# Optimization experiments

Measured on AMD Instinct MI355X. Metric: run time of the kernel, lower is better.

The kernel has to match this reference:

```python
import jax, jax.numpy as jnp
import numpy as np

LMAX, MMAX, C = 4, 2, 128
E, N = 40000, 4000
CUTOFF, RESCALE = 12.0, 5.0
EPS = 1e-5

def _mappings(lmax, mmax):
    # l-major coefficient listing with m in [-min(l,mmax), min(l,mmax)]
    m_list = []
    for l in range(lmax + 1):
        mm = min(l, mmax)
        m_list += list(range(-mm, mm + 1))
    m_c = np.array(m_list)
    n = len(m_list)
    to_m = np.zeros((n, n), dtype=np.float32)  # m-major <- l-major permutation
    off = 0
    for m in range(mmax + 1):
        idx_r = np.where(m_c == m)[0]
        for i, j in enumerate(idx_r):
            to_m[off + i, j] = 1.0
        off += len(idx_r)
        if m > 0:
            idx_i = np.where(m_c == -m)[0]
            for i, j in enumerate(idx_i):
                to_m[off + i, j] = 1.0
            off += len(idx_i)
    full_m = np.concatenate([np.arange(-l, l + 1) for l in range(lmax + 1)])
    out_idx = np.where(np.abs(full_m) <= mmax)[0]  # out_mask as index list
    return jnp.asarray(to_m), jnp.asarray(out_idx)

TO_M, OUT_IDX = _mappings(LMAX, MMAX)
M0 = LMAX + 1            # number of m=0 coefficients (5)
M_ALL = TO_M.shape[0]    # number of |m|<=mmax coefficients (19)
NCOEF = (LMAX + 1) ** 2  # full coefficient count (25)

def setup_inputs() -> dict:
    key = jax.random.key(0)
    ks = jax.random.split(key, 8)
    return {
        "x": jax.random.normal(ks[0], (N, NCOEF, C), jnp.float32),
        "x_edge": jax.random.normal(ks[1], (E, 128), jnp.float32),
        "edge_distance": jax.random.uniform(ks[2], (E,), jnp.float32) * CUTOFF,
        "wigner_inv": jax.random.normal(ks[3], (E, NCOEF, NCOEF), jnp.float32) / np.float32(np.sqrt(NCOEF)),
        "edge_index": jax.random.randint(ks[4], (2, E), 0, N),
        "w1": jax.random.normal(ks[5], (128, 64), jnp.float32) / np.float32(np.sqrt(128.0)),
        "b1": jnp.zeros((64,), jnp.float32),
        "g1": jnp.ones((64,), jnp.float32),
        "be1": jnp.zeros((64,), jnp.float32),
        "w2": jax.random.normal(ks[6], (64, 64), jnp.float32) / 8.0,
        "b2": jnp.zeros((64,), jnp.float32),
        "g2": jnp.ones((64,), jnp.float32),
        "be2": jnp.zeros((64,), jnp.float32),
        "w3": jax.random.normal(ks[7], (64, M0 * C), jnp.float32) / 8.0,
        "b3": jnp.zeros((M0 * C,), jnp.float32),
        "node_offset": 0,
    }

def _ln(h, g, b):
    mu = jnp.mean(h, -1, keepdims=True)
    var = jnp.mean((h - mu) ** 2, -1, keepdims=True)
    return (h - mu) * jax.lax.rsqrt(var + EPS) * g + b

def _envelope(d):
    # PolynomialEnvelope with exponent p=5
    p = 5.0
    a = -(p + 1.0) * (p + 2.0) / 2.0   # -21
    bb = p * (p + 2.0)                 #  35
    c = -p * (p + 1.0) / 2.0           # -15
    env = 1.0 + a * d**5 + bb * d**6 + c * d**7
    return jnp.where(d < 1.0, env, jnp.zeros_like(d))

def reference(x, x_edge, edge_distance, wigner_inv, edge_index,
              w1, b1, g1, be1, w2, b2, g2, be2, w3, b3, node_offset):
    # RadialMLP: (Linear -> LayerNorm -> SiLU) x2 -> Linear
    h = jax.nn.silu(_ln(x_edge @ w1 + b1, g1, be1))
    h = jax.nn.silu(_ln(h @ w2 + b2, g2, be2))
    m0 = (h @ w3 + b3).reshape(-1, M0, C)               # [E, M0, C]
    # zero-padding to M_ALL rows then applying the permutation TO_M equals
    # contracting only the first M0 (m=0) rows of TO_M
    emb = jnp.einsum("nac,ab->nbc", m0, TO_M[:M0])       # [E, M_ALL, C] (l-order)
    emb = jnp.einsum("nij,njc->nic", wigner_inv[:, :, OUT_IDX], emb)  # [E, NCOEF, C]
    env = _envelope(edge_distance / CUTOFF)
    emb = emb * env[:, None, None]
    dst = edge_index[1] - node_offset
    return x.at[dst].add(emb / RESCALE)
```

## Files before the change

kernel.cpp:

```cpp
#include <hip/hip_runtime.h>
#include <cstddef>


constexpr int C_DIM   = 128;
constexpr int NCOEF   = 25;
constexpr int M0d     = 5;
constexpr float EPS_LN      = 1e-5f;
constexpr float INV_CUTOFF  = 1.0f / 12.0f;
constexpr float INV_RESCALE = 0.2f;

typedef __attribute__((ext_vector_type(8))) short short8;
typedef __attribute__((ext_vector_type(4))) short short4v;
typedef __attribute__((ext_vector_type(4))) float f32x4;

__device__ __forceinline__ short f2bf(float f) {
    unsigned u = __float_as_uint(f);
    unsigned r = u + 0x7FFFu + ((u >> 16) & 1u);
    return (short)(r >> 16);
}

__device__ __forceinline__ float silu(float z) {
    return z / (1.0f + __expf(-z));
}

__global__ __launch_bounds__(256) void prep_weights(
    const float* __restrict__ w1, const float* __restrict__ w2,
    const float* __restrict__ w3,
    short* __restrict__ w1T, short* __restrict__ w2T, short* __restrict__ w3T)
{
    int i = blockIdx.x * 256 + threadIdx.x;
    if (i < 64 * 128) {
        int n = i >> 7, k = i & 127;
        w1T[i] = f2bf(w1[k * 64 + n]);
    }
    if (i < 64 * 64) {
        int n = i >> 6, k = i & 63;
        w2T[i] = f2bf(w2[k * 64 + n]);
    }
    if (i < 640 * 64) {
        int n = i >> 6, k = i & 63;
        w3T[i] = f2bf(w3[k * 640 + n]);
    }
}

__global__ __launch_bounds__(256) void count_kernel(
    const int* __restrict__ edge_index, const int* __restrict__ noff,
    int* __restrict__ cnt, int E, int N)
{
    int e = blockIdx.x * 256 + threadIdx.x;
    if (e < E) {
        int d = edge_index[E + e] - noff[0];
        if (d >= 0 && d < N) atomicAdd(&cnt[d], 1);
    }
}

__global__ __launch_bounds__(256) void scan_kernel(
    const int* __restrict__ cnt, int* __restrict__ offs, int N)
{
    __shared__ int s_wsum[4];
    const int t = threadIdx.x;
    const int lane = t & 63, w = t >> 6;
    const int chunk = (N + 255) / 256;
    const int base = t * chunk;

    int s = 0;
    for (int j = 0; j < chunk; ++j)
        if (base + j < N) s += cnt[base + j];

    int v = s;
    #pragma unroll
    for (int off = 1; off < 64; off <<= 1) {
        int u = __shfl_up(v, off, 64);
        if (lane >= off) v += u;
    }
    if (lane == 63) s_wsum[w] = v;
    __syncthreads();
    int wbase = 0;
    for (int k = 0; k < w; ++k) wbase += s_wsum[k];
    int run = wbase + v - s;

    if (t == 0) offs[0] = 0;
    for (int j = 0; j < chunk; ++j) {
        if (base + j < N) {
            run += cnt[base + j];
            offs[base + j + 1] = run;
        }
    }
}

__global__ __launch_bounds__(256) void fill_kernel(
    const int* __restrict__ edge_index, const int* __restrict__ noff,
    const int* __restrict__ offs, int* __restrict__ cur,
    int* __restrict__ ipos, int E, int N)
{
    int e = blockIdx.x * 256 + threadIdx.x;
    if (e < E) {
        int d = edge_index[E + e] - noff[0];
        if (d >= 0 && d < N) {
            int p = atomicAdd(&cur[d], 1);
            ipos[e] = offs[d] + p;
        }
    }
}

__global__ __launch_bounds__(256) void compact_kernel(
    const float* __restrict__ wigner_inv,
    const int*   __restrict__ ipos,
    unsigned short* __restrict__ wkT,
    int E)
{
    __shared__ float s_raw[16 * 625];
    __shared__ int   s_ipos[16];

    const int t  = threadIdx.x;
    const int g0 = blockIdx.x * 16;
    const int nloc = (E - g0) < 16 ? (E - g0) : 16;

    if (t < nloc) s_ipos[t] = ipos[g0 + t];

    if (nloc == 16) {
        const float4* src = (const float4*)(wigner_inv + (size_t)g0 * 625);
        #pragma unroll 4
        for (int f = t; f < 2500; f += 256)
            *(float4*)&s_raw[f * 4] = src[f];
    } else {
        const float* src = wigner_inv + (size_t)g0 * 625;
        for (int f = t; f < nloc * 625; f += 256)
            s_raw[f] = src[f];
    }
    __syncthreads();

    const int total = nloc * 160;
    #pragma unroll 4
    for (int f = t; f < total; f += 256) {
        int el = f / 160;
        int r  = f - el * 160;
        int a  = r >> 5;
        int i  = r & 31;
        int ip = s_ipos[el];
        if ((unsigned)ip < (unsigned)E) {
            unsigned short v = 0;
            if (i < 25) v = (unsigned short)f2bf(s_raw[el * 625 + i * 25 + a * (a + 1)]);
            wkT[((size_t)ip * 5 + a) * 32 + i] = v;
        }
    }
}

__global__ __launch_bounds__(256) void mlp_mfma_kernel(
    const float* __restrict__ x_edge,
    const float* __restrict__ edge_distance,
    const int*   __restrict__ ipos,
    const short* __restrict__ w1T,
    const float* __restrict__ b1,
    const float* __restrict__ g1, const float* __restrict__ be1,
    const short* __restrict__ w2T,
    const float* __restrict__ b2,
    const float* __restrict__ g2, const float* __restrict__ be2,
    const short* __restrict__ w3T,
    const float* __restrict__ b3,
    unsigned short* __restrict__ m0p,
    int E)
{
    __shared__ short s_h[4][1024];

    const int t  = threadIdx.x;
    const int w  = t >> 6;
    const int l  = t & 63;
    const int e16 = l & 15;
    const int g   = l >> 4;
    const int g0  = blockIdx.x * 64;
    const int row = g0 + w * 16 + e16;
    const int rowc = row < E ? row : (E - 1);
    const bool valid = row < E;
    const int swz = (e16 & 7) << 4;

    char* lds = (char*)&s_h[w][0];

    float sc;
    {
        float d  = edge_distance[rowc] * INV_CUTOFF;
        float d2 = d * d;
        float d5 = d2 * d2 * d;
        float env = 1.0f + d5 * (-21.0f + d * (35.0f + d * (-15.0f)));
        sc = ((d < 1.0f) ? env : 0.0f) * INV_RESCALE;
    }
    const int ip = valid ? ipos[rowc] : 0;
    const bool ipok = valid && ((unsigned)ip < (unsigned)E);

    short8 bx[4];
    {
        const float* xr = x_edge + (size_t)rowc * C_DIM + 8 * g;
        #pragma unroll
        for (int kt = 0; kt < 4; ++kt) {
            float4 f0 = *(const float4*)(xr + kt * 32);
            float4 f1 = *(const float4*)(xr + kt * 32 + 4);
            short8 v;
            v[0] = f2bf(f0.x); v[1] = f2bf(f0.y); v[2] = f2bf(f0.z); v[3] = f2bf(f0.w);
            v[4] = f2bf(f1.x); v[5] = f2bf(f1.y); v[6] = f2bf(f1.z); v[7] = f2bf(f1.w);
            bx[kt] = v;
        }
    }

    f32x4 acc1[4];
    #pragma unroll
    for (int nt = 0; nt < 4; ++nt) {
        float4 bv = *(const float4*)(b1 + nt * 16 + 4 * g);
        f32x4 acc = {bv.x, bv.y, bv.z, bv.w};
        #pragma unroll
        for (int kt = 0; kt < 4; ++kt) {
            short8 aw = *(const short8*)(w1T + (nt * 16 + e16) * 128 + kt * 32 + 8 * g);
            acc = __builtin_amdgcn_mfma_f32_16x16x32_bf16(aw, bx[kt], acc, 0, 0, 0);
        }
        acc1[nt] = acc;
    }

    {
        float s = 0.0f;
        #pragma unroll
        for (int nt = 0; nt < 4; ++nt)
            s += acc1[nt][0] + acc1[nt][1] + acc1[nt][2] + acc1[nt][3];
        s += __shfl_xor(s, 16);
        s += __shfl_xor(s, 32);
        float mu = s * (1.0f / 64.0f);
        float q = 0.0f;
        #pragma unroll
        for (int nt = 0; nt < 4; ++nt) {
            #pragma unroll
            for (int r = 0; r < 4; ++r) {
                float d = acc1[nt][r] - mu;
                q += d * d;
            }
        }
        q += __shfl_xor(q, 16);
        q += __shfl_xor(q, 32);
        float rstd = rsqrtf(q * (1.0f / 64.0f) + EPS_LN);
        #pragma unroll
        for (int nt = 0; nt < 4; ++nt) {
            float4 gv = *(const float4*)(g1 + nt * 16 + 4 * g);
            float4 bv = *(const float4*)(be1 + nt * 16 + 4 * g);
            short4v hv;
            hv[0] = f2bf(silu((acc1[nt][0] - mu) * rstd * gv.x + bv.x));
            hv[1] = f2bf(silu((acc1[nt][1] - mu) * rstd * gv.y + bv.y));
            hv[2] = f2bf(silu((acc1[nt][2] - mu) * rstd * gv.z + bv.z));
            hv[3] = f2bf(silu((acc1[nt][3] - mu) * rstd * gv.w + bv.w));
            *(short4v*)(lds + e16 * 128 + ((nt * 32 + 8 * g) ^ swz)) = hv;
        }
    }
    asm volatile("s_waitcnt lgkmcnt(0)" ::: "memory");

    short8 bh[2];
    #pragma unroll
    for (int kt = 0; kt < 2; ++kt)
        bh[kt] = *(const short8*)(lds + e16 * 128 + ((kt * 64 + 16 * g) ^ swz));

    f32x4 acc2[4];
    #pragma unroll
    for (int nt = 0; nt < 4; ++nt) {
        float4 bv = *(const float4*)(b2 + nt * 16 + 4 * g);
        f32x4 acc = {bv.x, bv.y, bv.z, bv.w};
        #pragma unroll
        for (int kt = 0; kt < 2; ++kt) {
            short8 aw = *(const short8*)(w2T + (nt * 16 + e16) * 64 + kt * 32 + 8 * g);
            acc = __builtin_amdgcn_mfma_f32_16x16x32_bf16(aw, bh[kt], acc, 0, 0, 0);
        }
        acc2[nt] = acc;
    }

    {
        float s = 0.0f;
        #pragma unroll
        for (int nt = 0; nt < 4; ++nt)
            s += acc2[nt][0] + acc2[nt][1] + acc2[nt][2] + acc2[nt][3];
        s += __shfl_xor(s, 16);
        s += __shfl_xor(s, 32);
        float mu = s * (1.0f / 64.0f);
        float q = 0.0f;
        #pragma unroll
        for (int nt = 0; nt < 4; ++nt) {
            #pragma unroll
            for (int r = 0; r < 4; ++r) {
                float d = acc2[nt][r] - mu;
                q += d * d;
            }
        }
        q += __shfl_xor(q, 16);
        q += __shfl_xor(q, 32);
        float rstd = rsqrtf(q * (1.0f / 64.0f) + EPS_LN);
        #pragma unroll
        for (int nt = 0; nt < 4; ++nt) {
            float4 gv = *(const float4*)(g2 + nt * 16 + 4 * g);
            float4 bv = *(const float4*)(be2 + nt * 16 + 4 * g);
            short4v hv;
            hv[0] = f2bf(silu((acc2[nt][0] - mu) * rstd * gv.x + bv.x));
            hv[1] = f2bf(silu((acc2[nt][1] - mu) * rstd * gv.y + bv.y));
            hv[2] = f2bf(silu((acc2[nt][2] - mu) * rstd * gv.z + bv.z));
            hv[3] = f2bf(silu((acc2[nt][3] - mu) * rstd * gv.w + bv.w));
            *(short4v*)(lds + e16 * 128 + ((nt * 32 + 8 * g) ^ swz)) = hv;
        }
    }
    asm volatile("s_waitcnt lgkmcnt(0)" ::: "memory");

    short8 bh2[2];
    #pragma unroll
    for (int kt = 0; kt < 2; ++kt)
        bh2[kt] = *(const short8*)(lds + e16 * 128 + ((kt * 64 + 16 * g) ^ swz));

    #pragma unroll 8
    for (int nt = 0; nt < 40; ++nt) {
        float4 bv = *(const float4*)(b3 + nt * 16 + 4 * g);
        f32x4 acc = {bv.x, bv.y, bv.z, bv.w};
        short8 aw0 = *(const short8*)(w3T + (nt * 16 + e16) * 64 + 8 * g);
        short8 aw1 = *(const short8*)(w3T + (nt * 16 + e16) * 64 + 32 + 8 * g);
        acc = __builtin_amdgcn_mfma_f32_16x16x32_bf16(aw0, bh2[0], acc, 0, 0, 0);
        acc = __builtin_amdgcn_mfma_f32_16x16x32_bf16(aw1, bh2[1], acc, 0, 0, 0);
        if (ipok) {
            short4v o;
            o[0] = f2bf(acc[0] * sc);
            o[1] = f2bf(acc[1] * sc);
            o[2] = f2bf(acc[2] * sc);
            o[3] = f2bf(acc[3] * sc);
            *(short4v*)(m0p + ((size_t)ip * 5 + (nt >> 3)) * 128
                            + ((nt & 7) << 4) + 4 * g) = o;
        }
    }
}

__global__ __launch_bounds__(256) void gather_mfma_kernel(
    const float* __restrict__ x,
    const unsigned short* __restrict__ m0p,
    const unsigned short* __restrict__ wkT,
    const int* __restrict__ offs,
    float* __restrict__ out, int N)
{
    const int n  = blockIdx.x;
    const int t  = threadIdx.x;
    const int w  = t >> 6;
    const int l  = t & 63;
    const int ln = l & 15;
    const int q  = l >> 4;
    const int myk = 8 * q;

    const int beg = offs[n], end = offs[n + 1];
    const int K = 5 * (end - beg);
    const size_t beg5 = (size_t)5 * beg;

    f32x4 acc[2][2];
    #pragma unroll
    for (int mt = 0; mt < 2; ++mt)
        #pragma unroll
        for (int bt = 0; bt < 2; ++bt)
            acc[mt][bt] = (f32x4){0.f, 0.f, 0.f, 0.f};

    const int nk = (K + 31) >> 5;
    for (int kt = 0; kt < nk; ++kt) {
        const int kb = kt * 32;
        const int limit = K - kb;
        const unsigned short* wrow = wkT + (beg5 + kb + myk) * 32 + ln;
        const unsigned short* mrow = m0p + (beg5 + kb + myk) * 128 + w * 32 + ln;

        short8 af[2], bf[2];
        if (limit >= 32) {
            #pragma unroll
            for (int j = 0; j < 8; ++j) {
                af[0][j] = (short)wrow[j * 32];
                af[1][j] = (short)wrow[j * 32 + 16];
                bf[0][j] = (short)mrow[j * 128];
                bf[1][j] = (short)mrow[j * 128 + 16];
            }
        } else {
            #pragma unroll
            for (int j = 0; j < 8; ++j) {
                const bool ok = (myk + j) < limit;
                af[0][j] = ok ? (short)wrow[j * 32] : (short)0;
                af[1][j] = ok ? (short)wrow[j * 32 + 16] : (short)0;
                bf[0][j] = ok ? (short)mrow[j * 128] : (short)0;
                bf[1][j] = ok ? (short)mrow[j * 128 + 16] : (short)0;
            }
        }

        #pragma unroll
        for (int mt = 0; mt < 2; ++mt)
            #pragma unroll
            for (int bt = 0; bt < 2; ++bt)
                acc[mt][bt] = __builtin_amdgcn_mfma_f32_16x16x32_bf16(
                    af[mt], bf[bt], acc[mt][bt], 0, 0, 0);
    }

    const size_t obase = (size_t)n * (NCOEF * C_DIM);
    #pragma unroll
    for (int mt = 0; mt < 2; ++mt) {
        #pragma unroll
        for (int r = 0; r < 4; ++r) {
            const int i = mt * 16 + 4 * q + r;
            if (i < NCOEF) {
                #pragma unroll
                for (int bt = 0; bt < 2; ++bt) {
                    const size_t idx = obase + (size_t)i * C_DIM + 32 * w + bt * 16 + ln;
                    out[idx] = x[idx] + acc[mt][bt][r];
                }
            }
        }
    }
}

constexpr int FEB = 8;
constexpr int BT  = 256;

__device__ __forceinline__ float ln_silu(float v, float g, float be) {
    float s = v;
    #pragma unroll
    for (int o = 32; o; o >>= 1) s += __shfl_xor(s, o, 64);
    float mu = s * (1.0f / 64.0f);
    float dv = v - mu;
    float q  = dv * dv;
    #pragma unroll
    for (int o = 32; o; o >>= 1) q += __shfl_xor(q, o, 64);
    float rstd = rsqrtf(q * (1.0f / 64.0f) + EPS_LN);
    float z = dv * rstd * g + be;
    return z / (1.0f + __expf(-z));
}

__global__ __launch_bounds__(BT) void edge_degree_fallback(
    const float* __restrict__ x_edge, const float* __restrict__ edge_distance,
    const float* __restrict__ wigner_inv, const int* __restrict__ edge_index,
    const float* __restrict__ w1, const float* __restrict__ b1,
    const float* __restrict__ g1, const float* __restrict__ be1,
    const float* __restrict__ w2, const float* __restrict__ b2,
    const float* __restrict__ g2, const float* __restrict__ be2,
    const float* __restrict__ w3, const float* __restrict__ b3,
    const int* __restrict__ node_offset_p, float* __restrict__ out, int E)
{
    __shared__ float s_xe[FEB][C_DIM];
    __shared__ float s_h1[FEB][64];
    __shared__ float s_h2[FEB][64];
    __shared__ float s_wig[FEB][NCOEF * M0d];
    __shared__ float s_scale[FEB];
    __shared__ int   s_dst[FEB];

    const int t = threadIdx.x;
    const int g0 = blockIdx.x * FEB;
    const int ne = (E - g0) < FEB ? (E - g0) : FEB;

    {
        const float* src = x_edge + (size_t)g0 * C_DIM;
        for (int f = t; f < FEB * C_DIM; f += BT) {
            int e = f >> 7;
            ((float*)s_xe)[f] = (e < ne) ? src[f] : 0.0f;
        }
    }
    {
        const int wcol_[M0d] = {0, 2, 6, 12, 20};
        for (int f = t; f < FEB * NCOEF * M0d; f += BT) {
            int e = f / 125, r = f - e * 125, i = r / 5, a = r - i * 5;
            float v = 0.0f;
            if (e < ne)
                v = wigner_inv[((size_t)(g0 + e)) * (NCOEF * NCOEF) + i * NCOEF + wcol_[a]];
            s_wig[e][r] = v;
        }
    }
    if (t < FEB) {
        if (t < ne) {
            float d = edge_distance[g0 + t] * INV_CUTOFF;
            float d2 = d * d, d5 = d2 * d2 * d;
            float env = 1.0f + d5 * (-21.0f + d * (35.0f + d * (-15.0f)));
            s_scale[t] = ((d < 1.0f) ? env : 0.0f) * INV_RESCALE;
            s_dst[t] = edge_index[E + g0 + t] - node_offset_p[0];
        } else { s_scale[t] = 0.0f; s_dst[t] = 0; }
    }
    __syncthreads();

    const int wv = t >> 6, j = t & 63;
    {
        float acc0 = b1[j], acc1 = acc0;
        for (int k = 0; k < C_DIM; ++k) {
            float w = w1[k * 64 + j];
            acc0 += s_xe[wv][k] * w;
            acc1 += s_xe[wv + 4][k] * w;
        }
        const float g = g1[j], be = be1[j];
        s_h1[wv][j]     = ln_silu(acc0, g, be);
        s_h1[wv + 4][j] = ln_silu(acc1, g, be);
    }
    __syncthreads();
    {
        float acc0 = b2[j], acc1 = acc0;
        for (int k = 0; k < 64; ++k) {
            float w = w2[k * 64 + j];
            acc0 += s_h1[wv][k] * w;
            acc1 += s_h1[wv + 4][k] * w;
        }
        const float g = g2[j], be = be2[j];
        s_h2[wv][j]     = ln_silu(acc0, g, be);
        s_h2[wv + 4][j] = ln_silu(acc1, g, be);
    }
    __syncthreads();

    const int c = t & 127, half = t >> 7;
    float m0r[4][M0d];
    #pragma unroll
    for (int a = 0; a < M0d; ++a) {
        float bb = b3[a * C_DIM + c];
        float a0 = bb, a1 = bb, a2 = bb, a3 = bb;
        const float* w3c = w3 + a * C_DIM + c;
        for (int k = 0; k < 64; ++k) {
            float w = w3c[k * (M0d * C_DIM)];
            a0 += s_h2[half + 0][k] * w;
            a1 += s_h2[half + 2][k] * w;
            a2 += s_h2[half + 4][k] * w;
            a3 += s_h2[half + 6][k] * w;
        }
        m0r[0][a] = a0; m0r[1][a] = a1; m0r[2][a] = a2; m0r[3][a] = a3;
    }
    #pragma unroll
    for (int ei = 0; ei < 4; ++ei) {
        const int e = half + 2 * ei;
        if (e >= ne) continue;
        const float sc = s_scale[e];
        float* obase = out + (size_t)s_dst[e] * (NCOEF * C_DIM) + c;
        #pragma unroll
        for (int i = 0; i < NCOEF; ++i) {
            const float* wg = &s_wig[e][i * M0d];
            float v = wg[0] * m0r[ei][0] + wg[1] * m0r[ei][1] + wg[2] * m0r[ei][2]
                    + wg[3] * m0r[ei][3] + wg[4] * m0r[ei][4];
            atomicAdd(obase + i * C_DIM, v * sc);
        }
    }
}

extern "C" void kernel_launch(void* const* d_in, const int* in_sizes, int n_in,
                              void* d_out, int out_size, void* d_ws, size_t ws_size,
                              hipStream_t stream)
{
    const float* x             = (const float*)d_in[0];
    const float* x_edge        = (const float*)d_in[1];
    const float* edge_distance = (const float*)d_in[2];
    const float* wigner_inv    = (const float*)d_in[3];
    const int*   edge_index    = (const int*)d_in[4];
    const float* w1  = (const float*)d_in[5];
    const float* b1  = (const float*)d_in[6];
    const float* g1  = (const float*)d_in[7];
    const float* be1 = (const float*)d_in[8];
    const float* w2  = (const float*)d_in[9];
    const float* b2  = (const float*)d_in[10];
    const float* g2  = (const float*)d_in[11];
    const float* be2 = (const float*)d_in[12];
    const float* w3  = (const float*)d_in[13];
    const float* b3  = (const float*)d_in[14];
    const int*   node_offset = (const int*)d_in[15];

    float* out = (float*)d_out;
    const int E = in_sizes[1] / C_DIM;
    const int N = in_sizes[0] / (NCOEF * C_DIM);
    const size_t KROWS = (size_t)5 * E + 32;

    size_t off = 0;
    const size_t m0p_off  = off; off += KROWS * 128 * 2;
    const size_t wkT_off  = off; off += KROWS * 32 * 2;
    const size_t cnt_off  = off; off += (size_t)N * 4;
    const size_t cur_off  = off; off += (size_t)N * 4;
    const size_t offs_off = off; off += (size_t)(N + 1) * 4;
    const size_t ipos_off = off; off += (size_t)E * 4;
    off = (off + 255) & ~(size_t)255;
    const size_t w1T_off  = off; off += 64 * 128 * 2;
    const size_t w2T_off  = off; off += 64 * 64 * 2;
    const size_t w3T_off  = off; off += 640 * 64 * 2;
    const size_t need     = off;

    if (ws_size >= need) {
        char* ws   = (char*)d_ws;
        unsigned short* m0p = (unsigned short*)(ws + m0p_off);
        unsigned short* wkT = (unsigned short*)(ws + wkT_off);
        int* cnt   = (int*)(ws + cnt_off);
        int* cur   = (int*)(ws + cur_off);
        int* offs  = (int*)(ws + offs_off);
        int* ipos  = (int*)(ws + ipos_off);
        short* w1T = (short*)(ws + w1T_off);
        short* w2T = (short*)(ws + w2T_off);
        short* w3T = (short*)(ws + w3T_off);

        hipMemsetAsync(cnt, 0, (size_t)N * 8, stream);

        prep_weights<<<(640 * 64 + 255) / 256, 256, 0, stream>>>(w1, w2, w3, w1T, w2T, w3T);
        count_kernel<<<(E + 255) / 256, 256, 0, stream>>>(edge_index, node_offset, cnt, E, N);
        scan_kernel<<<1, 256, 0, stream>>>(cnt, offs, N);
        fill_kernel<<<(E + 255) / 256, 256, 0, stream>>>(edge_index, node_offset, offs, cur, ipos, E, N);

        compact_kernel<<<(E + 15) / 16, 256, 0, stream>>>(wigner_inv, ipos, wkT, E);

        mlp_mfma_kernel<<<(E + 63) / 64, 256, 0, stream>>>(
            x_edge, edge_distance, ipos,
            w1T, b1, g1, be1, w2T, b2, g2, be2, w3T, b3, m0p, E);

        gather_mfma_kernel<<<N, 256, 0, stream>>>(x, m0p, wkT, offs, out, N);
    } else {
        hipMemcpyAsync(out, x, (size_t)out_size * sizeof(float),
                       hipMemcpyDeviceToDevice, stream);
        edge_degree_fallback<<<(E + FEB - 1) / FEB, BT, 0, stream>>>(
            x_edge, edge_distance, wigner_inv, edge_index,
            w1, b1, g1, be1, w2, b2, g2, be2, w3, b3,
            node_offset, out, E);
    }
}
```

Measured before the change: 136.5 us.

## Split MLP N-dimension across waves and gather m0 rows via permutation

The MLP kernel now processes 16 edges per block, with each of the four waves computing a 16-column slice of every layer. LayerNorm statistics are combined across waves through shared memory and barriers. The m=0 outputs are written in edge order, and the gather kernel reads them indirectly through a new perm array (dst-sorted position to edge), cached in LDS. The memset is replaced by a small zero kernel. This aims to raise MLP parallelism and coalesce its stores, at the cost of extra barriers, 4x more blocks and scattered indirect reads in the gather.

After: 151.4 us. 10.9% more time.

```diff
diff --git a/kernel.cpp b/kernel.cpp
--- a/kernel.cpp
+++ b/kernel.cpp
@@ -23,6 +23,11 @@
     return z / (1.0f + __expf(-z));
 }
 
+__global__ __launch_bounds__(256) void zero_kernel(int* __restrict__ p, int n) {
+    int i = blockIdx.x * 256 + threadIdx.x;
+    if (i < n) p[i] = 0;
+}
+
 __global__ __launch_bounds__(256) void prep_weights(
     const float* __restrict__ w1, const float* __restrict__ w2,
     const float* __restrict__ w3,
@@ -91,14 +96,16 @@
 __global__ __launch_bounds__(256) void fill_kernel(
     const int* __restrict__ edge_index, const int* __restrict__ noff,
     const int* __restrict__ offs, int* __restrict__ cur,
-    int* __restrict__ ipos, int E, int N)
+    int* __restrict__ perm, int* __restrict__ ipos, int E, int N)
 {
     int e = blockIdx.x * 256 + threadIdx.x;
     if (e < E) {
         int d = edge_index[E + e] - noff[0];
         if (d >= 0 && d < N) {
             int p = atomicAdd(&cur[d], 1);
-            ipos[e] = offs[d] + p;
+            int pos = offs[d] + p;
+            perm[pos] = e;
+            ipos[e]   = pos;
         }
     }
 }
@@ -149,7 +156,6 @@
 __global__ __launch_bounds__(256) void mlp_mfma_kernel(
     const float* __restrict__ x_edge,
     const float* __restrict__ edge_distance,
-    const int*   __restrict__ ipos,
     const short* __restrict__ w1T,
     const float* __restrict__ b1,
     const float* __restrict__ g1, const float* __restrict__ be1,
@@ -158,23 +164,26 @@
     const float* __restrict__ g2, const float* __restrict__ be2,
     const short* __restrict__ w3T,
     const float* __restrict__ b3,
-    unsigned short* __restrict__ m0p,
+    unsigned short* __restrict__ m0s,
     int E)
 {
-    __shared__ short s_h[4][1024];
-
-    const int t  = threadIdx.x;
-    const int w  = t >> 6;
-    const int l  = t & 63;
+    __shared__ float s_part[128];
+    __shared__ short sh1[1024];
+    __shared__ short sh2[1024];
+
+    const int t   = threadIdx.x;
+    const int w   = t >> 6;
+    const int l   = t & 63;
     const int e16 = l & 15;
     const int g   = l >> 4;
-    const int g0  = blockIdx.x * 64;
-    const int row = g0 + w * 16 + e16;
+    const int g0  = (int)blockIdx.x * 16;
+    const int row = g0 + e16;
     const int rowc = row < E ? row : (E - 1);
     const bool valid = row < E;
     const int swz = (e16 & 7) << 4;
 
-    char* lds = (char*)&s_h[w][0];
+    char* sh1b = (char*)sh1;
+    char* sh2b = (char*)sh2;
 
     float sc;
     {
@@ -184,8 +193,6 @@
         float env = 1.0f + d5 * (-21.0f + d * (35.0f + d * (-15.0f)));
         sc = ((d < 1.0f) ? env : 0.0f) * INV_RESCALE;
     }
-    const int ip = valid ? ipos[rowc] : 0;
-    const bool ipok = valid && ((unsigned)ip < (unsigned)E);
 
     short8 bx[4];
     {
@@ -201,137 +208,123 @@
         }
     }
 
-    f32x4 acc1[4];
-    #pragma unroll
-    for (int nt = 0; nt < 4; ++nt) {
-        float4 bv = *(const float4*)(b1 + nt * 16 + 4 * g);
-        f32x4 acc = {bv.x, bv.y, bv.z, bv.w};
+    f32x4 acc1;
+    {
+        float4 bv = *(const float4*)(b1 + w * 16 + 4 * g);
+        acc1 = (f32x4){bv.x, bv.y, bv.z, bv.w};
         #pragma unroll
         for (int kt = 0; kt < 4; ++kt) {
-            short8 aw = *(const short8*)(w1T + (nt * 16 + e16) * 128 + kt * 32 + 8 * g);
-            acc = __builtin_amdgcn_mfma_f32_16x16x32_bf16(aw, bx[kt], acc, 0, 0, 0);
-        }
-        acc1[nt] = acc;
-    }
-
-    {
-        float s = 0.0f;
-        #pragma unroll
-        for (int nt = 0; nt < 4; ++nt)
-            s += acc1[nt][0] + acc1[nt][1] + acc1[nt][2] + acc1[nt][3];
+            short8 aw = *(const short8*)(w1T + (w * 16 + e16) * 128 + kt * 32 + 8 * g);
+            acc1 = __builtin_amdgcn_mfma_f32_16x16x32_bf16(aw, bx[kt], acc1, 0, 0, 0);
+        }
+    }
+
+    {
+        float s = acc1[0] + acc1[1] + acc1[2] + acc1[3];
         s += __shfl_xor(s, 16);
         s += __shfl_xor(s, 32);
-        float mu = s * (1.0f / 64.0f);
+        if (g == 0) s_part[w * 16 + e16] = s;
+        __syncthreads();
+        float mu = (s_part[e16] + s_part[16 + e16] + s_part[32 + e16] + s_part[48 + e16])
+                   * (1.0f / 64.0f);
         float q = 0.0f;
         #pragma unroll
-        for (int nt = 0; nt < 4; ++nt) {
-            #pragma unroll
-            for (int r = 0; r < 4; ++r) {
-                float d = acc1[nt][r] - mu;
-                q += d * d;
-            }
-        }
+        for (int r = 0; r < 4; ++r) { float d = acc1[r] - mu; q += d * d; }
         q += __shfl_xor(q, 16);
         q += __shfl_xor(q, 32);
-        float rstd = rsqrtf(q * (1.0f / 64.0f) + EPS_LN);
-        #pragma unroll
-        for (int nt = 0; nt < 4; ++nt) {
-            float4 gv = *(const float4*)(g1 + nt * 16 + 4 * g);
-            float4 bv = *(const float4*)(be1 + nt * 16 + 4 * g);
-            short4v hv;
-            hv[0] = f2bf(silu((acc1[nt][0] - mu) * rstd * gv.x + bv.x));
-            hv[1] = f2bf(silu((acc1[nt][1] - mu) * rstd * gv.y + bv.y));
-            hv[2] = f2bf(silu((acc1[nt][2] - mu) * rstd * gv.z + bv.z));
-            hv[3] = f2bf(silu((acc1[nt][3] - mu) * rstd * gv.w + bv.w));
-            *(short4v*)(lds + e16 * 128 + ((nt * 32 + 8 * g) ^ swz)) = hv;
-        }
-    }
-    asm volatile("s_waitcnt lgkmcnt(0)" ::: "memory");
-
-    short8 bh[2];
-    #pragma unroll
-    for (int kt = 0; kt < 2; ++kt)
-        bh[kt] = *(const short8*)(lds + e16 * 128 + ((kt * 64 + 16 * g) ^ swz));
-
-    f32x4 acc2[4];
-    #pragma unroll
-    for (int nt = 0; nt < 4; ++nt) {
-        float4 bv = *(const float4*)(b2 + nt * 16 + 4 * g);
-        f32x4 acc = {bv.x, bv.y, bv.z, bv.w};
+        if (g == 0) s_part[64 + w * 16 + e16] = q;
+        __syncthreads();
+        float qt = s_part[64 + e16] + s_part[80 + e16] + s_part[96 + e16] + s_part[112 + e16];
+        float rstd = rsqrtf(qt * (1.0f / 64.0f) + EPS_LN);
+        float4 gv = *(const float4*)(g1 + w * 16 + 4 * g);
+        float4 bv = *(const float4*)(be1 + w * 16 + 4 * g);
+        short4v hv;
+        hv[0] = f2bf(silu((acc1[0] - mu) * rstd * gv.x + bv.x));
+        hv[1] = f2bf(silu((acc1[1] - mu) * rstd * gv.y + bv.y));
+        hv[2] = f2bf(silu((acc1[2] - mu) * rstd * gv.z + bv.z));
+        hv[3] = f2bf(silu((acc1[3] - mu) * rstd * gv.w + bv.w));
+        *(short4v*)(sh1b + e16 * 128 + ((w * 32 + 8 * g) ^ swz)) = hv;
+        __syncthreads();
+    }
+
+    f32x4 acc2;
+    {
+        short8 bh[2];
+        #pragma unroll
+        for (int kt = 0; kt < 2; ++kt)
+            bh[kt] = *(const short8*)(sh1b + e16 * 128 + ((kt * 64 + 16 * g) ^ swz));
+        float4 bv = *(const float4*)(b2 + w * 16 + 4 * g);
+        acc2 = (f32x4){bv.x, bv.y, bv.z, bv.w};
         #pragma unroll
         for (int kt = 0; kt < 2; ++kt) {
-            short8 aw = *(const short8*)(w2T + (nt * 16 + e16) * 64 + kt * 32 + 8 * g);
-            acc = __builtin_amdgcn_mfma_f32_16x16x32_bf16(aw, bh[kt], acc, 0, 0, 0);
-        }
-        acc2[nt] = acc;
-    }
-
-    {
-        float s = 0.0f;
-        #pragma unroll
-        for (int nt = 0; nt < 4; ++nt)
-            s += acc2[nt][0] + acc2[nt][1] + acc2[nt][2] + acc2[nt][3];
+            short8 aw = *(const short8*)(w2T + (w * 16 + e16) * 64 + kt * 32 + 8 * g);
+            acc2 = __builtin_amdgcn_mfma_f32_16x16x32_bf16(aw, bh[kt], acc2, 0, 0, 0);
+        }
+    }
+
+    {
+        float s = acc2[0] + acc2[1] + acc2[2] + acc2[3];
         s += __shfl_xor(s, 16);
         s += __shfl_xor(s, 32);
-        float mu = s * (1.0f / 64.0f);
+        if (g == 0) s_part[w * 16 + e16] = s;
+        __syncthreads();
+        float mu = (s_part[e16] + s_part[16 + e16] + s_part[32 + e16] + s_part[48 + e16])
+                   * (1.0f / 64.0f);
         float q = 0.0f;
         #pragma unroll
-        for (int nt = 0; nt < 4; ++nt) {
-            #pragma unroll
-            for (int r = 0; r < 4; ++r) {
-                float d = acc2[nt][r] - mu;
-                q += d * d;
-            }
-        }
+        for (int r = 0; r < 4; ++r) { float d = acc2[r] - mu; q += d * d; }
         q += __shfl_xor(q, 16);
         q += __shfl_xor(q, 32);
-        float rstd = rsqrtf(q * (1.0f / 64.0f) + EPS_LN);
-        #pragma unroll
-        for (int nt = 0; nt < 4; ++nt) {
-            float4 gv = *(const float4*)(g2 + nt * 16 + 4 * g);
-            float4 bv = *(const float4*)(be2 + nt * 16 + 4 * g);
-            short4v hv;
-            hv[0] = f2bf(silu((acc2[nt][0] - mu) * rstd * gv.x + bv.x));
-            hv[1] = f2bf(silu((acc2[nt][1] - mu) * rstd * gv.y + bv.y));
-            hv[2] = f2bf(silu((acc2[nt][2] - mu) * rstd * gv.z + bv.z));
-            hv[3] = f2bf(silu((acc2[nt][3] - mu) * rstd * gv.w + bv.w));
-            *(short4v*)(lds + e16 * 128 + ((nt * 32 + 8 * g) ^ swz)) = hv;
-        }
-    }
-    asm volatile("s_waitcnt lgkmcnt(0)" ::: "memory");
+        if (g == 0) s_part[64 + w * 16 + e16] = q;
+        __syncthreads();
+        float qt = s_part[64 + e16] + s_part[80 + e16] + s_part[96 + e16] + s_part[112 + e16];
+        float rstd = rsqrtf(qt * (1.0f / 64.0f) + EPS_LN);
+        float4 gv = *(const float4*)(g2 + w * 16 + 4 * g);
+        float4 bv = *(const float4*)(be2 + w * 16 + 4 * g);
+        short4v hv;
+        hv[0] = f2bf(silu((acc2[0] - mu) * rstd * gv.x + bv.x));
+        hv[1] = f2bf(silu((acc2[1] - mu) * rstd * gv.y + bv.y));
+        hv[2] = f2bf(silu((acc2[2] - mu) * rstd * gv.z + bv.z));
+        hv[3] = f2bf(silu((acc2[3] - mu) * rstd * gv.w + bv.w));
+        *(short4v*)(sh2b + e16 * 128 + ((w * 32 + 8 * g) ^ swz)) = hv;
+        __syncthreads();
+    }
 
     short8 bh2[2];
     #pragma unroll
     for (int kt = 0; kt < 2; ++kt)
-        bh2[kt] = *(const short8*)(lds + e16 * 128 + ((kt * 64 + 16 * g) ^ swz));
-
-    #pragma unroll 8
-    for (int nt = 0; nt < 40; ++nt) {
+        bh2[kt] = *(const short8*)(sh2b + e16 * 128 + ((kt * 64 + 16 * g) ^ swz));
+
+    unsigned short* orow = m0s + (size_t)row * 640 + 4 * g;
+    #pragma unroll 5
+    for (int j = 0; j < 10; ++j) {
+        const int nt = w * 10 + j;
         float4 bv = *(const float4*)(b3 + nt * 16 + 4 * g);
         f32x4 acc = {bv.x, bv.y, bv.z, bv.w};
         short8 aw0 = *(const short8*)(w3T + (nt * 16 + e16) * 64 + 8 * g);
         short8 aw1 = *(const short8*)(w3T + (nt * 16 + e16) * 64 + 32 + 8 * g);
         acc = __builtin_amdgcn_mfma_f32_16x16x32_bf16(aw0, bh2[0], acc, 0, 0, 0);
         acc = __builtin_amdgcn_mfma_f32_16x16x32_bf16(aw1, bh2[1], acc, 0, 0, 0);
-        if (ipok) {
+        if (valid) {
             short4v o;
             o[0] = f2bf(acc[0] * sc);
             o[1] = f2bf(acc[1] * sc);
             o[2] = f2bf(acc[2] * sc);
             o[3] = f2bf(acc[3] * sc);
-            *(short4v*)(m0p + ((size_t)ip * 5 + (nt >> 3)) * 128
-                            + ((nt & 7) << 4) + 4 * g) = o;
+            *(short4v*)(orow + nt * 16) = o;
         }
     }
 }
 
 __global__ __launch_bounds__(256) void gather_mfma_kernel(
     const float* __restrict__ x,
-    const unsigned short* __restrict__ m0p,
+    const unsigned short* __restrict__ m0s,
     const unsigned short* __restrict__ wkT,
-    const int* __restrict__ offs,
+    const int* __restrict__ perm, const int* __restrict__ offs,
     float* __restrict__ out, int N)
 {
+    __shared__ int s_perm5[512];
+
     const int n  = blockIdx.x;
     const int t  = threadIdx.x;
     const int w  = t >> 6;
@@ -341,8 +334,13 @@
     const int myk = 8 * q;
 
     const int beg = offs[n], end = offs[n + 1];
-    const int K = 5 * (end - beg);
+    const int cnt = end - beg;
+    const int K = 5 * cnt;
     const size_t beg5 = (size_t)5 * beg;
+
+    for (int p = t; p < cnt && p < 512; p += 256)
+        s_perm5[p] = perm[beg + p] * 5;
+    __syncthreads();
 
     f32x4 acc[2][2];
     #pragma unroll
@@ -356,25 +354,25 @@
         const int kb = kt * 32;
         const int limit = K - kb;
         const unsigned short* wrow = wkT + (beg5 + kb + myk) * 32 + ln;
-        const unsigned short* mrow = m0p + (beg5 + kb + myk) * 128 + w * 32 + ln;
+        const int cbase = w * 32 + ln;
 
         short8 af[2], bf[2];
-        if (limit >= 32) {
-            #pragma unroll
-            for (int j = 0; j < 8; ++j) {
-                af[0][j] = (short)wrow[j * 32];
-                af[1][j] = (short)wrow[j * 32 + 16];
-                bf[0][j] = (short)mrow[j * 128];
-                bf[1][j] = (short)mrow[j * 128 + 16];
-            }
-        } else {
-            #pragma unroll
-            for (int j = 0; j < 8; ++j) {
-                const bool ok = (myk + j) < limit;
-                af[0][j] = ok ? (short)wrow[j * 32] : (short)0;
-                af[1][j] = ok ? (short)wrow[j * 32 + 16] : (short)0;
-                bf[0][j] = ok ? (short)mrow[j * 128] : (short)0;
-                bf[1][j] = ok ? (short)mrow[j * 128 + 16] : (short)0;
+        #pragma unroll
+        for (int j = 0; j < 8; ++j) {
+            const int kl = kb + myk + j;
+            const bool ok = kl < K;
+            af[0][j] = ok ? (short)wrow[j * 32] : (short)0;
+            af[1][j] = ok ? (short)wrow[j * 32 + 16] : (short)0;
+            if (ok) {
+                const int pos = kl / 5;
+                const int a   = kl - pos * 5;
+                const int e5  = (pos < 512) ? s_perm5[pos] : perm[beg + pos] * 5;
+                const unsigned short* mrow = m0s + (size_t)(e5 + a) * 128 + cbase;
+                bf[0][j] = (short)mrow[0];
+                bf[1][j] = (short)mrow[16];
+            } else {
+                bf[0][j] = 0;
+                bf[1][j] = 0;
             }
         }
 
@@ -554,11 +552,12 @@
     const size_t KROWS = (size_t)5 * E + 32;
 
     size_t off = 0;
-    const size_t m0p_off  = off; off += KROWS * 128 * 2;
+    const size_t m0_off   = off; off += (size_t)E * 640 * 2;
     const size_t wkT_off  = off; off += KROWS * 32 * 2;
     const size_t cnt_off  = off; off += (size_t)N * 4;
     const size_t cur_off  = off; off += (size_t)N * 4;
     const size_t offs_off = off; off += (size_t)(N + 1) * 4;
+    const size_t perm_off = off; off += (size_t)E * 4;
     const size_t ipos_off = off; off += (size_t)E * 4;
     off = (off + 255) & ~(size_t)255;
     const size_t w1T_off  = off; off += 64 * 128 * 2;
@@ -568,30 +567,31 @@
 
     if (ws_size >= need) {
         char* ws   = (char*)d_ws;
-        unsigned short* m0p = (unsigned short*)(ws + m0p_off);
+        unsigned short* m0s = (unsigned short*)(ws + m0_off);
         unsigned short* wkT = (unsigned short*)(ws + wkT_off);
         int* cnt   = (int*)(ws + cnt_off);
         int* cur   = (int*)(ws + cur_off);
         int* offs  = (int*)(ws + offs_off);
+        int* perm  = (int*)(ws + perm_off);
         int* ipos  = (int*)(ws + ipos_off);
         short* w1T = (short*)(ws + w1T_off);
         short* w2T = (short*)(ws + w2T_off);
         short* w3T = (short*)(ws + w3T_off);
 
-        hipMemsetAsync(cnt, 0, (size_t)N * 8, stream);
+        zero_kernel<<<(2 * N + 255) / 256, 256, 0, stream>>>(cnt, 2 * N);
 
         prep_weights<<<(640 * 64 + 255) / 256, 256, 0, stream>>>(w1, w2, w3, w1T, w2T, w3T);
         count_kernel<<<(E + 255) / 256, 256, 0, stream>>>(edge_index, node_offset, cnt, E, N);
         scan_kernel<<<1, 256, 0, stream>>>(cnt, offs, N);
-        fill_kernel<<<(E + 255) / 256, 256, 0, stream>>>(edge_index, node_offset, offs, cur, ipos, E, N);
+        fill_kernel<<<(E + 255) / 256, 256, 0, stream>>>(edge_index, node_offset, offs, cur, perm, ipos, E, N);
 
         compact_kernel<<<(E + 15) / 16, 256, 0, stream>>>(wigner_inv, ipos, wkT, E);
 
-        mlp_mfma_kernel<<<(E + 63) / 64, 256, 0, stream>>>(
-            x_edge, edge_distance, ipos,
-            w1T, b1, g1, be1, w2T, b2, g2, be2, w3T, b3, m0p, E);
-
-        gather_mfma_kernel<<<N, 256, 0, stream>>>(x, m0p, wkT, offs, out, N);
+        mlp_mfma_kernel<<<(E + 15) / 16, 256, 0, stream>>>(
+            x_edge, edge_distance,
+            w1T, b1, g1, be1, w2T, b2, g2, be2, w3T, b3, m0s, E);
+
+        gather_mfma_kernel<<<N, 256, 0, stream>>>(x, m0s, wkT, perm, offs, out, N);
     } else {
         hipMemcpyAsync(out, x, (size_t)out_size * sizeof(float),
                        hipMemcpyDeviceToDevice, stream);
```
